# Kernel optimization log

Measured on AMD Instinct MI355X. Metric: run time of the kernel, lower is better.

Reference implementation:

```python
import jax, jax.numpy as jnp
import numpy as np

N = 50000
E = 1600000
F_IN = 128
C_OUT = 64
HEADS = 2
NEG_SLOPE = 0.2
EPS = 1e-5


def setup_inputs() -> dict:
    key = jax.random.key(0)
    ks = jax.random.split(key, 8)
    HC = HEADS * C_OUT
    glorot = lambda k, shape: jax.random.normal(k, shape, jnp.float32) * np.sqrt(2.0 / (shape[0] + shape[-1]))
    return {
        "x": jax.random.normal(ks[0], (N, F_IN), jnp.float32),
        "edge_index": jax.random.randint(ks[1], (2, E), 0, N, jnp.int64),
        "W_l": glorot(ks[2], (F_IN, HC)),
        "W_r": glorot(ks[3], (F_IN, HC)),
        "att": glorot(ks[4], (HEADS, C_OUT)),
        "bias": jnp.zeros((HC,), jnp.float32),
        "gn_weight": jnp.ones((HC,), jnp.float32),
        "gn_bias": jnp.zeros((HC,), jnp.float32),
        "gn_mean_scale": jnp.ones((HC,), jnp.float32),
    }


def reference(x, edge_index, W_l, W_r, att, bias, gn_weight, gn_bias, gn_mean_scale):
    n = x.shape[0]
    # --- GATv2Conv (share_weights=False, concat=True, dropout=0) ---
    x_l = (x @ W_l).reshape(n, HEADS, C_OUT)  # source transform
    x_r = (x @ W_r).reshape(n, HEADS, C_OUT)  # target transform
    # add self loops
    loop = jnp.arange(n, dtype=edge_index.dtype)
    src = jnp.concatenate([edge_index[0], loop])
    dst = jnp.concatenate([edge_index[1], loop])
    # edge-wise attention logits: LeakyReLU(x_l[j] + x_r[i]) . att
    xs = x_l[src] + x_r[dst]  # [E', H, C]
    e = jax.nn.leaky_relu(xs, NEG_SLOPE)
    logits = jnp.einsum('ehc,hc->eh', e, att)  # [E', H]
    # segment softmax over edges sharing the same target node
    seg_max = jax.ops.segment_max(logits, dst, num_segments=n)  # [N, H]
    exp = jnp.exp(logits - seg_max[dst])
    seg_sum = jax.ops.segment_sum(exp, dst, num_segments=n)
    alpha = exp / seg_sum[dst]  # [E', H]
    # scatter-aggregate messages
    msg = alpha[:, :, None] * x_l[src]  # [E', H, C]
    out = jax.ops.segment_sum(msg, dst, num_segments=n)  # [N, H, C]
    out = out.reshape(n, HEADS * C_OUT) + bias
    # --- GraphNorm (single graph) ---
    mean = out.mean(axis=0)
    centered = out - mean * gn_mean_scale
    var = (centered * centered).mean(axis=0)
    return gn_weight * centered / jnp.sqrt(var + EPS) + gn_bias
```

## Files before the change

kernel.cpp:

```cpp
#include <hip/hip_runtime.h>
#include <math.h>

#define NEG_SLOPE 0.2f
#define GN_EPS 1e-5f
#define NBSHIFT 8
#define CHUNK 2048

typedef _Float16 h2 __attribute__((ext_vector_type(2)));
typedef _Float16 half8 __attribute__((ext_vector_type(8)));
typedef float f32x4 __attribute__((ext_vector_type(4)));

__device__ __forceinline__ int rfl(int v) {
  return __builtin_amdgcn_readfirstlane(v);
}

template <int PAT>
__device__ __forceinline__ float swz(float v) {
  return __builtin_bit_cast(
      float, (unsigned)__builtin_amdgcn_ds_swizzle(__builtin_bit_cast(int, v),
                                                   PAT));
}

__device__ __forceinline__ unsigned int pkh(float a, float b) {
  return __builtin_bit_cast(unsigned int, __builtin_amdgcn_cvt_pkrtz(a, b));
}

__device__ __forceinline__ h2 bch2(unsigned int u) {
  return __builtin_bit_cast(h2, u);
}

__device__ __forceinline__ h2 mkh2(float a, float b) {
  return __builtin_bit_cast(h2, __builtin_amdgcn_cvt_pkrtz(a, b));
}

__device__ __forceinline__ float dot2f(h2 a, h2 b, float c) {
#if __has_builtin(__builtin_amdgcn_fdot2)
  return __builtin_amdgcn_fdot2(a, b, c, false);
#else
  return fmaf((float)a.x, (float)b.x, fmaf((float)a.y, (float)b.y, c));
#endif
}

__device__ __forceinline__ float lkdot(h2 xl, h2 xr, h2 a, float p) {
  h2 t = xl + xr;
  h2 z = {(_Float16)0.f, (_Float16)0.f};
#if __has_builtin(__builtin_elementwise_min)
  h2 mn = __builtin_elementwise_min(t, z);
#else
  h2 mn;
  mn.x = (t.x < z.x) ? t.x : z.x;
  mn.y = (t.y < z.y) ? t.y : z.y;
#endif
  h2 km1 = {(_Float16)(NEG_SLOPE - 1.0f), (_Float16)(NEG_SLOPE - 1.0f)};
  h2 g = mn * km1 + t;
  return dot2f(g, a, p);
}

__global__ __launch_bounds__(256) void gemm_hist(
    const float* __restrict__ x, const float* __restrict__ Wl,
    const float* __restrict__ Wr, unsigned int* __restrict__ xlb,
    unsigned int* __restrict__ xrh, int n, const int* __restrict__ ei,
    int* __restrict__ bhist, int e, int gemm_blocks) {
  if ((int)blockIdx.x >= gemm_blocks) {
    __shared__ int hist[256];
    hist[threadIdx.x] = 0;
    __syncthreads();
    const int nbk = gridDim.x - gemm_blocks;
    const int stride = nbk * 256;
    for (int i = ((int)blockIdx.x - gemm_blocks) * 256 + threadIdx.x; i < e;
         i += stride)
      atomicAdd(&hist[ei[e + i] >> NBSHIFT], 1);
    __syncthreads();
    int v = hist[threadIdx.x];
    if (v > 0) atomicAdd(&bhist[threadIdx.x], v);
    return;
  }

  const int wv = threadIdx.x >> 6;
  const int lane = threadIdx.x & 63;
  const int lr = lane & 15;
  const int lk = lane >> 4;
  const int node0 = (int)blockIdx.x * 64;
  const float* __restrict__ Wp = (wv < 2) ? Wl : Wr;
  unsigned int* __restrict__ dst = (wv < 2) ? xlb : xrh;
  const int chBase = (wv & 1) * 64;

  f32x4 acc[4][4];
#pragma unroll
  for (int mt = 0; mt < 4; ++mt)
#pragma unroll
    for (int nt = 0; nt < 4; ++nt) acc[mt][nt] = (f32x4){0.f, 0.f, 0.f, 0.f};

  int nd[4];
#pragma unroll
  for (int nt = 0; nt < 4; ++nt) nd[nt] = min(node0 + nt * 16 + lr, n - 1);

#pragma unroll
  for (int kc = 0; kc < 4; ++kc) {
    const int k0 = kc * 32 + lk * 8;
    half8 a[4];
#pragma unroll
    for (int mt = 0; mt < 4; ++mt) {
      const float* __restrict__ wp =
          Wp + (size_t)k0 * 128 + chBase + mt * 16 + lr;
      float w0 = wp[0 * 128], w1 = wp[1 * 128], w2 = wp[2 * 128],
            w3 = wp[3 * 128];
      float w4 = wp[4 * 128], w5 = wp[5 * 128], w6 = wp[6 * 128],
            w7 = wp[7 * 128];
      uint4 ua;
      ua.x = pkh(w0, w1);
      ua.y = pkh(w2, w3);
      ua.z = pkh(w4, w5);
      ua.w = pkh(w6, w7);
      a[mt] = __builtin_bit_cast(half8, ua);
    }
    half8 b[4];
#pragma unroll
    for (int nt = 0; nt < 4; ++nt) {
      const float4 f0 = *(const float4*)(x + (size_t)nd[nt] * 128 + k0);
      const float4 f1 = *(const float4*)(x + (size_t)nd[nt] * 128 + k0 + 4);
      uint4 ub;
      ub.x = pkh(f0.x, f0.y);
      ub.y = pkh(f0.z, f0.w);
      ub.z = pkh(f1.x, f1.y);
      ub.w = pkh(f1.z, f1.w);
      b[nt] = __builtin_bit_cast(half8, ub);
    }
#pragma unroll
    for (int mt = 0; mt < 4; ++mt)
#pragma unroll
      for (int nt = 0; nt < 4; ++nt)
        acc[mt][nt] = __builtin_amdgcn_mfma_f32_16x16x32_f16(
            a[mt], b[nt], acc[mt][nt], 0, 0, 0);
  }

  const int dw0 = (chBase >> 1) + lk * 2;
#pragma unroll
  for (int nt = 0; nt < 4; ++nt) {
    const int node = node0 + nt * 16 + lr;
    if (node >= n) continue;
#pragma unroll
    for (int mt = 0; mt < 4; ++mt) {
      uint2 p;
      p.x = pkh(acc[mt][nt][0], acc[mt][nt][1]);
      p.y = pkh(acc[mt][nt][2], acc[mt][nt][3]);
      *(uint2*)(dst + (size_t)node * 64 + dw0 + mt * 8) = p;
    }
  }
}

__global__ __launch_bounds__(256) void bscan(const int* __restrict__ bhist,
                                             int* __restrict__ bbase,
                                             int* __restrict__ gcur,
                                             int* __restrict__ offsets, int nb,
                                             int n, int e) {
  __shared__ int sd[256];
  int t = threadIdx.x;
  int v = (t < nb) ? bhist[t] : 0;
  sd[t] = v;
  __syncthreads();
#pragma unroll
  for (int s = 1; s < 256; s <<= 1) {
    int add = (t >= s) ? sd[t - s] : 0;
    __syncthreads();
    sd[t] += add;
    __syncthreads();
  }
  int excl = sd[t] - v;
  if (t < nb) {
    bbase[t] = excl;
    gcur[t] = excl;
  } else {
    gcur[t] = 0;
  }
  if (t == 0) {
    bbase[nb] = e;
    offsets[n] = e;
  }
}

__global__ __launch_bounds__(256) void partition(const int* __restrict__ ei,
                                                 int* __restrict__ gcur,
                                                 unsigned int* __restrict__ ebuf,
                                                 int e) {
  __shared__ unsigned int ent[CHUNK];
  __shared__ int hist[256];
  __shared__ int lcur[256];
  const int t = threadIdx.x;
  const int c0 = blockIdx.x * CHUNK;
  const int cend = min(c0 + CHUNK, e);
  hist[t] = 0;
  __syncthreads();
  for (int i = c0 + t; i < cend; i += 256) {
    const int dst = ei[e + i];
    const int src = ei[i];
    const int b = dst >> NBSHIFT;
    atomicAdd(&hist[b], 1);
    ent[i - c0] = (unsigned int)src | ((unsigned int)(dst & 255) << 16) |
                  ((unsigned int)b << 24);
  }
  __syncthreads();
  lcur[t] = atomicAdd(&gcur[t], hist[t]);
  __syncthreads();
  for (int i = c0 + t; i < cend; i += 256) {
    const unsigned int u = ent[i - c0];
    const int b = u >> 24;
    int pos = atomicAdd(&lcur[b], 1);
    ebuf[pos] = u;
  }
}

__global__ __launch_bounds__(1024) void csr_build(
    const unsigned int* __restrict__ ebuf, const int* __restrict__ bbase,
    int* __restrict__ offsets, unsigned short* __restrict__ csr16, int n) {
  __shared__ int hist[256];
  __shared__ int sc[256];
  const int b = blockIdx.x;
  const int t = threadIdx.x;
  const int node0 = b << NBSHIFT;
  const int seg0 = bbase[b];
  const int seg1 = bbase[b + 1];

  if (t < 256) hist[t] = 0;
  __syncthreads();
  for (int i = seg0 + t; i < seg1; i += 1024)
    atomicAdd(&hist[(ebuf[i] >> 16) & 255], 1);
  __syncthreads();
  int v = 0;
  if (t < 256) {
    v = hist[t];
    sc[t] = v;
  }
  __syncthreads();
#pragma unroll
  for (int s = 1; s < 256; s <<= 1) {
    int add = (t >= s && t < 256) ? sc[t - s] : 0;
    __syncthreads();
    if (t < 256) sc[t] += add;
    __syncthreads();
  }
  if (t < 256) {
    int start = seg0 + sc[t] - v;
    int node = node0 + t;
    if (node < n) offsets[node] = start;
    hist[t] = start;
  }
  __syncthreads();
  for (int i = seg0 + t; i < seg1; i += 1024) {
    unsigned int u = ebuf[i];
    int pos = atomicAdd(&hist[(u >> 16) & 255], 1);
    csr16[pos] = (unsigned short)(u & 0xFFFFu);
  }
}

__global__ __launch_bounds__(256) void node_agg(
    const unsigned int* __restrict__ xlh, const unsigned int* __restrict__ xrh,
    const int* __restrict__ offsets, const unsigned short* __restrict__ csr16,
    const float* __restrict__ att, const float* __restrict__ bias,
    float* __restrict__ out, int n) {
  const int wave = threadIdx.x >> 6;
  const int lane = threadIdx.x & 63;
  const int node = blockIdx.x * 4 + wave;
  if (node >= n) return;
  const int q = lane >> 4;
  const int r = lane & 15;

  const uint4 xr4 = *(const uint4*)(xrh + (size_t)node * 64 + r * 4);
  const h2 xr0 = bch2(xr4.x), xr1 = bch2(xr4.y), xr2v = bch2(xr4.z),
           xr3 = bch2(xr4.w);
  const float4 a0 = *(const float4*)(att + r * 8);
  const float4 a1 = *(const float4*)(att + r * 8 + 4);
  const h2 ah0 = mkh2(a0.x, a0.y), ah1 = mkh2(a0.z, a0.w),
           ah2 = mkh2(a1.x, a1.y), ah3 = mkh2(a1.z, a1.w);

  const int start = rfl(offsets[node]);
  const int end = rfl(offsets[node + 1]);
  const int deg = end - start;
  const int T = deg + 1;

  float s = 0.f;
  float accf[8];
#pragma unroll
  for (int i = 0; i < 8; ++i) accf[i] = 0.f;

  const char* __restrict__ xlbase = (const char*)xlh;
  const unsigned roff = (unsigned)(r * 16);

  auto gat = [&](int src) {
    return *(const uint4*)(xlbase + (((unsigned)src << 8) | roff));
  };

  auto quadp = [&](uint4 xl4, bool valid) {
    const h2 x0 = bch2(xl4.x), x1 = bch2(xl4.y), x2 = bch2(xl4.z),
             x3 = bch2(xl4.w);
    float p = 0.f;
    p = lkdot(x0, xr0, ah0, p);
    p = lkdot(x1, xr1, ah1, p);
    p = lkdot(x2, xr2v, ah2, p);
    p = lkdot(x3, xr3, ah3, p);
    p += swz<0x041F>(p);
    p += swz<0x081F>(p);
    p += swz<0x101F>(p);
    const float w = valid ? __expf(p) : 0.f;
    s += w;
    accf[0] = fmaf((float)x0.x, w, accf[0]);
    accf[1] = fmaf((float)x0.y, w, accf[1]);
    accf[2] = fmaf((float)x1.x, w, accf[2]);
    accf[3] = fmaf((float)x1.y, w, accf[3]);
    accf[4] = fmaf((float)x2.x, w, accf[4]);
    accf[5] = fmaf((float)x2.y, w, accf[5]);
    accf[6] = fmaf((float)x3.x, w, accf[6]);
    accf[7] = fmaf((float)x3.y, w, accf[7]);
  };

  for (int b0 = 0; b0 < T; b0 += 64) {
    const int m = min(64, T - b0);
    const int kk = b0 + lane;
    const int cl = min(kk, T - 1);
    int idx = node;
    if (deg > 0) {
      idx = csr16[start + max(cl - 1, 0)];
      if (cl == 0) idx = node;
    }
    int j = 0;
    for (; j + 16 <= m; j += 16) {
      const int s0 = __shfl(idx, j + q, 64);
      const int s1 = __shfl(idx, j + 4 + q, 64);
      const int s2 = __shfl(idx, j + 8 + q, 64);
      const int s3 = __shfl(idx, j + 12 + q, 64);
      const uint4 g0 = gat(s0);
      const uint4 g1 = gat(s1);
      const uint4 g2 = gat(s2);
      const uint4 g3 = gat(s3);
      quadp(g0, true);
      quadp(g1, true);
      quadp(g2, true);
      quadp(g3, true);
    }
    for (; j + 4 <= m; j += 4)
      quadp(gat(__shfl(idx, j + q, 64)), true);
    if (j < m) {
      const int eo = j + q;
      quadp(gat(__shfl(idx, min(eo, m - 1), 64)), eo < m);
    }
  }

  s += swz<0x401F>(s);
  s += __shfl_xor(s, 32, 64);
#pragma unroll
  for (int i = 0; i < 8; ++i) {
    accf[i] += swz<0x401F>(accf[i]);
    accf[i] += __shfl_xor(accf[i], 32, 64);
  }

  if (q == 0) {
    const float inv = 1.f / s;
    const float4 b0v = *(const float4*)(bias + r * 8);
    const float4 b1v = *(const float4*)(bias + r * 8 + 4);
    float4 o0 = make_float4(fmaf(accf[0], inv, b0v.x), fmaf(accf[1], inv, b0v.y),
                            fmaf(accf[2], inv, b0v.z), fmaf(accf[3], inv, b0v.w));
    float4 o1 = make_float4(fmaf(accf[4], inv, b1v.x), fmaf(accf[5], inv, b1v.y),
                            fmaf(accf[6], inv, b1v.z), fmaf(accf[7], inv, b1v.w));
    *(float4*)(out + (size_t)node * 128 + r * 8) = o0;
    *(float4*)(out + (size_t)node * 128 + r * 8 + 4) = o1;
  }
}

__global__ __launch_bounds__(256) void gn_partial(const float4* __restrict__ out4,
                                                  float* __restrict__ part,
                                                  int total4) {
  const int t = threadIdx.x;
  float s0 = 0.f, s1 = 0.f, s2 = 0.f, s3 = 0.f;
  float q0 = 0.f, q1 = 0.f, q2 = 0.f, q3 = 0.f;
  const int stride = gridDim.x * 256;
  for (int i = blockIdx.x * 256 + t; i < total4; i += stride) {
    float4 v = out4[i];
    s0 += v.x; q0 = fmaf(v.x, v.x, q0);
    s1 += v.y; q1 = fmaf(v.y, v.y, q1);
    s2 += v.z; q2 = fmaf(v.z, v.z, q2);
    s3 += v.w; q3 = fmaf(v.w, v.w, q3);
  }
  __shared__ float red[8][128];
  const int row = t >> 5;
  const int cb = (t & 31) * 4;
  *(float4*)&red[row][cb] = make_float4(s0, s1, s2, s3);
  __syncthreads();
  if (t < 128) {
    float S = 0.f;
#pragma unroll
    for (int r = 0; r < 8; ++r) S += red[r][t];
    part[blockIdx.x * 256 + t] = S;
  }
  __syncthreads();
  *(float4*)&red[row][cb] = make_float4(q0, q1, q2, q3);
  __syncthreads();
  if (t < 128) {
    float Q = 0.f;
#pragma unroll
    for (int r = 0; r < 8; ++r) Q += red[r][t];
    part[blockIdx.x * 256 + 128 + t] = Q;
  }
}

__global__ __launch_bounds__(1024) void gn_final(const float* __restrict__ part,
                                                 const float* __restrict__ gw,
                                                 const float* __restrict__ gb,
                                                 const float* __restrict__ gms,
                                                 float* __restrict__ AB,
                                                 int nblocks, float inv_n) {
  __shared__ float sS[8][128];
  __shared__ float sQ[8][128];
  const int c = threadIdx.x & 127;
  const int sl = threadIdx.x >> 7;
  float S = 0.f, Q = 0.f;
#pragma unroll 8
  for (int b = sl; b < nblocks; b += 8) {
    S += part[b * 256 + c];
    Q += part[b * 256 + 128 + c];
  }
  sS[sl][c] = S;
  sQ[sl][c] = Q;
  __syncthreads();
  if (sl == 0) {
#pragma unroll
    for (int i = 1; i < 8; ++i) {
      S += sS[i][c];
      Q += sQ[i][c];
    }
    float mean = S * inv_n;
    float msc = mean * gms[c];
    float var = Q * inv_n - 2.f * msc * mean + msc * msc;
    float scale = gw[c] * rsqrtf(var + GN_EPS);
    AB[c] = scale;
    AB[128 + c] = gb[c] - scale * msc;
  }
}

__global__ void gn_apply(float* __restrict__ out, const float* __restrict__ AB,
                         int total4) {
  int i = blockIdx.x * blockDim.x + threadIdx.x;
  if (i >= total4) return;
  float4 v = ((float4*)out)[i];
  int c4 = (i & 31) * 4;
  v.x = fmaf(AB[c4 + 0], v.x, AB[128 + c4 + 0]);
  v.y = fmaf(AB[c4 + 1], v.y, AB[128 + c4 + 1]);
  v.z = fmaf(AB[c4 + 2], v.z, AB[128 + c4 + 2]);
  v.w = fmaf(AB[c4 + 3], v.w, AB[128 + c4 + 3]);
  ((float4*)out)[i] = v;
}

extern "C" void kernel_launch(void* const* d_in, const int* in_sizes, int n_in,
                              void* d_out, int out_size, void* d_ws,
                              size_t ws_size, hipStream_t stream) {
  const float* x = (const float*)d_in[0];
  const int* ei = (const int*)d_in[1];
  const float* Wl = (const float*)d_in[2];
  const float* Wr = (const float*)d_in[3];
  const float* att = (const float*)d_in[4];
  const float* bias = (const float*)d_in[5];
  const float* gw = (const float*)d_in[6];
  const float* gb = (const float*)d_in[7];
  const float* gms = (const float*)d_in[8];
  float* out = (float*)d_out;

  const int n = in_sizes[0] / 128;
  const int e = in_sizes[1] / 2;
  const int nb = (n + 255) >> NBSHIFT;
  const int nchunks = (e + CHUNK - 1) / CHUNK;
  const int GN_BLOCKS = 512;
  const int gemm_blocks = (n + 63) / 64;
  const int hist_blocks = 196;

  char* w = (char*)d_ws;
  auto alloc = [&](size_t bytes) {
    char* p = w;
    w += (bytes + 255) & ~(size_t)255;
    return p;
  };
  unsigned int* xlb = (unsigned int*)alloc((size_t)n * 64 * sizeof(int));
  unsigned int* xrh = (unsigned int*)alloc((size_t)n * 64 * sizeof(int));
  int* offsets = (int*)alloc((size_t)(n + 1) * sizeof(int));
  unsigned short* csr16 =
      (unsigned short*)alloc((size_t)e * sizeof(unsigned short));
  unsigned int* ebuf = (unsigned int*)alloc((size_t)e * sizeof(int));
  int* bhist = (int*)alloc(256 * sizeof(int));
  int* bbase = (int*)alloc((size_t)(nb + 1) * sizeof(int));
  int* gcur = (int*)alloc(256 * sizeof(int));
  float* part = (float*)alloc((size_t)GN_BLOCKS * 256 * sizeof(float));
  float* AB = (float*)alloc(256 * sizeof(float));

  hipMemsetAsync(bhist, 0, 256 * sizeof(int), stream);

  gemm_hist<<<gemm_blocks + hist_blocks, 256, 0, stream>>>(
      x, Wl, Wr, xlb, xrh, n, ei, bhist, e, gemm_blocks);
  bscan<<<1, 256, 0, stream>>>(bhist, bbase, gcur, offsets, nb, n, e);
  partition<<<nchunks, 256, 0, stream>>>(ei, gcur, ebuf, e);
  csr_build<<<nb, 1024, 0, stream>>>(ebuf, bbase, offsets, csr16, n);
  node_agg<<<(n + 3) / 4, 256, 0, stream>>>(xlb, xrh, offsets, csr16, att,
                                            bias, out, n);
  gn_partial<<<GN_BLOCKS, 256, 0, stream>>>((const float4*)out, part, n * 32);
  gn_final<<<1, 1024, 0, stream>>>(part, gw, gb, gms, AB, GN_BLOCKS,
                                   1.0f / (float)n);
  gn_apply<<<(n * 32 + 255) / 256, 256, 0, stream>>>(out, AB, n * 32);
}
```

Baseline: 238.7 us.

## Precompute packed fp16 weight fragments and split node aggregation into two launches

Adds a small kernel that converts W_l and W_r to fp16 once and packs them in MFMA fragment order. The GEMM waves then load one uint4 per tile instead of eight strided float loads plus conversions in every block. Separately, node_agg is split into two launches, each covering half the nodes. The split adds a launch and does not obviously reduce any cost, and the weight packing adds an extra kernel launch of its own.

```diff
diff --git a/kernel.cpp b/kernel.cpp
--- a/kernel.cpp
+++ b/kernel.cpp
@@ -56,11 +56,36 @@
   return dot2f(g, a, p);
 }
 
+__global__ __launch_bounds__(256) void wconv(const float* __restrict__ Wl,
+                                             const float* __restrict__ Wr,
+                                             uint4* __restrict__ whf) {
+  const int tid = blockIdx.x * 256 + threadIdx.x;
+  const int m = tid >> 11;
+  const int rem = tid & 2047;
+  const int h = rem >> 10;
+  const int kc = (rem >> 8) & 3;
+  const int mt = (rem >> 6) & 3;
+  const int lk = (rem >> 4) & 3;
+  const int lr = rem & 15;
+  const int k0 = kc * 32 + lk * 8;
+  const int col = h * 64 + mt * 16 + lr;
+  const float* __restrict__ W = m ? Wr : Wl;
+  const float* __restrict__ wp = W + (size_t)k0 * 128 + col;
+  float w0 = wp[0 * 128], w1 = wp[1 * 128], w2 = wp[2 * 128], w3 = wp[3 * 128];
+  float w4 = wp[4 * 128], w5 = wp[5 * 128], w6 = wp[6 * 128], w7 = wp[7 * 128];
+  uint4 u;
+  u.x = pkh(w0, w1);
+  u.y = pkh(w2, w3);
+  u.z = pkh(w4, w5);
+  u.w = pkh(w6, w7);
+  whf[tid] = u;
+}
+
 __global__ __launch_bounds__(256) void gemm_hist(
-    const float* __restrict__ x, const float* __restrict__ Wl,
-    const float* __restrict__ Wr, unsigned int* __restrict__ xlb,
-    unsigned int* __restrict__ xrh, int n, const int* __restrict__ ei,
-    int* __restrict__ bhist, int e, int gemm_blocks) {
+    const float* __restrict__ x, const uint4* __restrict__ whf,
+    unsigned int* __restrict__ xlb, unsigned int* __restrict__ xrh, int n,
+    const int* __restrict__ ei, int* __restrict__ bhist, int e,
+    int gemm_blocks) {
   if ((int)blockIdx.x >= gemm_blocks) {
     __shared__ int hist[256];
     hist[threadIdx.x] = 0;
@@ -81,9 +106,9 @@
   const int lr = lane & 15;
   const int lk = lane >> 4;
   const int node0 = (int)blockIdx.x * 64;
-  const float* __restrict__ Wp = (wv < 2) ? Wl : Wr;
   unsigned int* __restrict__ dst = (wv < 2) ? xlb : xrh;
   const int chBase = (wv & 1) * 64;
+  const uint4* __restrict__ wf = whf + ((wv >= 2) ? 2048 : 0) + (wv & 1) * 1024;
 
   f32x4 acc[4][4];
 #pragma unroll
@@ -100,20 +125,8 @@
     const int k0 = kc * 32 + lk * 8;
     half8 a[4];
 #pragma unroll
-    for (int mt = 0; mt < 4; ++mt) {
-      const float* __restrict__ wp =
-          Wp + (size_t)k0 * 128 + chBase + mt * 16 + lr;
-      float w0 = wp[0 * 128], w1 = wp[1 * 128], w2 = wp[2 * 128],
-            w3 = wp[3 * 128];
-      float w4 = wp[4 * 128], w5 = wp[5 * 128], w6 = wp[6 * 128],
-            w7 = wp[7 * 128];
-      uint4 ua;
-      ua.x = pkh(w0, w1);
-      ua.y = pkh(w2, w3);
-      ua.z = pkh(w4, w5);
-      ua.w = pkh(w6, w7);
-      a[mt] = __builtin_bit_cast(half8, ua);
-    }
+    for (int mt = 0; mt < 4; ++mt)
+      a[mt] = __builtin_bit_cast(half8, wf[kc * 256 + mt * 64 + lane]);
     half8 b[4];
 #pragma unroll
     for (int nt = 0; nt < 4; ++nt) {
@@ -257,11 +270,11 @@
     const unsigned int* __restrict__ xlh, const unsigned int* __restrict__ xrh,
     const int* __restrict__ offsets, const unsigned short* __restrict__ csr16,
     const float* __restrict__ att, const float* __restrict__ bias,
-    float* __restrict__ out, int n) {
+    float* __restrict__ out, int base, int nend) {
   const int wave = threadIdx.x >> 6;
   const int lane = threadIdx.x & 63;
-  const int node = blockIdx.x * 4 + wave;
-  if (node >= n) return;
+  const int node = base + blockIdx.x * 4 + wave;
+  if (node >= nend) return;
   const int q = lane >> 4;
   const int r = lane & 15;
 
@@ -483,6 +496,7 @@
   unsigned short* csr16 =
       (unsigned short*)alloc((size_t)e * sizeof(unsigned short));
   unsigned int* ebuf = (unsigned int*)alloc((size_t)e * sizeof(int));
+  uint4* whf = (uint4*)alloc(4096 * sizeof(uint4));
   int* bhist = (int*)alloc(256 * sizeof(int));
   int* bbase = (int*)alloc((size_t)(nb + 1) * sizeof(int));
   int* gcur = (int*)alloc(256 * sizeof(int));
@@ -491,13 +505,17 @@
 
   hipMemsetAsync(bhist, 0, 256 * sizeof(int), stream);
 
+  wconv<<<16, 256, 0, stream>>>(Wl, Wr, whf);
   gemm_hist<<<gemm_blocks + hist_blocks, 256, 0, stream>>>(
-      x, Wl, Wr, xlb, xrh, n, ei, bhist, e, gemm_blocks);
+      x, whf, xlb, xrh, n, ei, bhist, e, gemm_blocks);
   bscan<<<1, 256, 0, stream>>>(bhist, bbase, gcur, offsets, nb, n, e);
   partition<<<nchunks, 256, 0, stream>>>(ei, gcur, ebuf, e);
   csr_build<<<nb, 1024, 0, stream>>>(ebuf, bbase, offsets, csr16, n);
-  node_agg<<<(n + 3) / 4, 256, 0, stream>>>(xlb, xrh, offsets, csr16, att,
-                                            bias, out, n);
+  const int half = ((n / 2) + 3) & ~3;
+  node_agg<<<(half + 3) / 4, 256, 0, stream>>>(xlb, xrh, offsets, csr16, att,
+                                               bias, out, 0, half);
+  node_agg<<<((n - half) + 3) / 4, 256, 0, stream>>>(xlb, xrh, offsets, csr16,
+                                                     att, bias, out, half, n);
   gn_partial<<<GN_BLOCKS, 256, 0, stream>>>((const float4*)out, part, n * 32);
   gn_final<<<1, 1024, 0, stream>>>(part, gw, gb, gms, AB, GN_BLOCKS,
                                    1.0f / (float)n);
```

Result: no change. 241.2 us (+1.0%).
